# Kernel optimization log

Hardware: AMD Instinct MI355X
Metric: run time of the kernel (lower is better)

## Reference

```python
import jax, jax.numpy as jnp
import numpy as np

N, CIN, COUT, V, T, S = 32, 64, 128, 25, 300, 3  # batch, in/out channels, joints, frames, subsets
EPS = 1e-5  # torch BatchNorm2d default eps


def setup_inputs() -> dict:
    key = jax.random.key(0)
    ks = jax.random.split(key, 16)
    f = lambda i, shape, sc=1.0: jax.random.normal(ks[i], shape, jnp.float32) * sc
    return dict(
        x=f(0, (N, CIN, V, T)),            # forward arg: input features
        ada_A=f(1, (N, CIN, V, V), 0.1),   # forward arg: adaptive adjacency features
        PA=f(2, (S, V, V), 0.1),           # learned adjacency (adaptive=True)
        conv3_w=f(3, (S, COUT, CIN), 0.05),  # per-subset 1x1 conv weights
        conv3_b=f(4, (S, COUT), 0.01),
        ada_w=f(5, (S, COUT, CIN), 0.05),    # per-subset conv_ada weights
        ada_b=f(6, (S, COUT), 0.01),
        bn_gamma=jnp.ones((COUT,), jnp.float32),
        bn_beta=jnp.zeros((COUT,), jnp.float32),
        bn_mean=f(7, (COUT,), 0.01),
        bn_var=jnp.abs(f(8, (COUT,))) + 1.0,
        down_w=f(9, (COUT, CIN), 0.05),      # residual 1x1 conv (in_c != out_c)
        down_b=f(10, (COUT,), 0.01),
        dbn_gamma=jnp.ones((COUT,), jnp.float32),
        dbn_beta=jnp.zeros((COUT,), jnp.float32),
        dbn_mean=f(11, (COUT,), 0.01),
        dbn_var=jnp.abs(f(12, (COUT,))) + 1.0,
    )


def _bn(y, g, b, m, v):
    # inference-mode BatchNorm2d over channel axis 1; y: [N, C, V, T]
    scale = g * jax.lax.rsqrt(v + EPS)
    return (y - m[:, None, None]) * scale[:, None, None] + b[:, None, None]


def reference(x, ada_A, PA, conv3_w, conv3_b, ada_w, ada_b,
              bn_gamma, bn_beta, bn_mean, bn_var,
              down_w, down_b, dbn_gamma, dbn_beta, dbn_mean, dbn_var):
    # per-subset 1x1 conv on features: feat[s] = conv3_s(x)  -> [S, N, COUT, V, T]
    feat = jnp.einsum('nivt,soi->snovt', x, conv3_w) + conv3_b[:, None, :, None, None]
    # per-subset 1x1 conv on adjacency features -> [S, N, COUT, V, V]
    adaA = jnp.einsum('nivw,soi->snovw', ada_A, ada_w) + ada_b[:, None, :, None, None]
    # modulate by learned adjacency PA[s] broadcast over (batch, channel)
    A_full = adaA * PA[:, None, None, :, :]
    # graph matmul per subset + sum over subsets -> [N, COUT, V, T]
    out = jnp.einsum('snovw,snowt->novt', A_full, feat)
    out = _bn(out, bn_gamma, bn_beta, bn_mean, bn_var)
    # residual down-path: 1x1 conv + BN (in_c != out_c)
    res = jnp.einsum('nivt,oi->novt', x, down_w) + down_b[:, None, None]
    res = _bn(res, dbn_gamma, dbn_beta, dbn_mean, dbn_var)
    return jax.nn.relu(out + res)
```

## Files before the change

### kernel.cpp

```cpp
#include <hip/hip_runtime.h>
#include <stdint.h>

#define N_    32
#define CIN_  64
#define COUT_ 128
#define V_    25
#define T_    300
#define S_    3


using short8 = __attribute__((ext_vector_type(8))) short;
using f32x4  = __attribute__((ext_vector_type(4))) float;

#define MFMA(a, b, c) __builtin_amdgcn_mfma_f32_16x16x32_bf16(a, b, c, 0, 0, 0)

__device__ __forceinline__ float b2f(unsigned short u) {
  return __uint_as_float(((uint32_t)u) << 16);
}
__device__ __forceinline__ unsigned short f2b(float f) {
  uint32_t u = __float_as_uint(f);
  u += 0x7fffu + ((u >> 16) & 1u);
  return (unsigned short)(u >> 16);
}
template<bool ISB>
__device__ __forceinline__ float ldf(const void* p, int i) {
  return ISB ? b2f(((const unsigned short*)p)[i]) : ((const float*)p)[i];
}
__device__ __forceinline__ short8 zero8() {
  short8 z = {0, 0, 0, 0, 0, 0, 0, 0};
  return z;
}
__device__ __forceinline__ short8 ld_s8(const unsigned short* p, int st) {
  union { uint32_t u[4]; short8 s; } r;
  r.u[0] = (uint32_t)p[0]      | ((uint32_t)p[st]     << 16);
  r.u[1] = (uint32_t)p[2 * st] | ((uint32_t)p[3 * st] << 16);
  r.u[2] = (uint32_t)p[4 * st] | ((uint32_t)p[5 * st] << 16);
  r.u[3] = (uint32_t)p[6 * st] | ((uint32_t)p[7 * st] << 16);
  return r.s;
}
__device__ __forceinline__ short8 ld_f8h(const float* p, int st) {
  short8 r;
#pragma unroll
  for (int j = 0; j < 8; ++j) r[j] = (short)f2b(p[j * st]);
  return r;
}
__device__ __forceinline__ void ld_f8s(const float* p, int st,
                                       short8& h, short8& l) {
#pragma unroll
  for (int j = 0; j < 8; ++j) {
    float xv = p[j * st];
    unsigned short hu = f2b(xv);
    h[j] = (short)hu;
    l[j] = (short)f2b(xv - b2f(hu));
  }
}

__global__ void gcn_dtype_flag(const void* __restrict__ gamma, int* __restrict__ flag) {
  if (threadIdx.x == 0 && blockIdx.x == 0)
    flag[0] = (((const unsigned short*)gamma)[0] == 0x3F80u) ? 1 : 0;
}

__global__ __launch_bounds__(256) void tx_bf(
    const unsigned short* __restrict__ x, unsigned short* __restrict__ xt,
    const int* __restrict__ flag) {
  if (!flag || flag[0] == 0) return;
  __shared__ uint32_t til[64][151];
  const int b = blockIdx.x, n = b / 25, v = b % 25, tid = threadIdx.x;
  const unsigned short* xp = x + (size_t)n * 480000 + v * 300;
  for (int u = tid; u < 9600; u += 256) {
    const int i = u / 150, tp = u % 150;
    til[i][tp] = *(const uint32_t*)(xp + (size_t)i * 7500 + 2 * tp);
  }
  __syncthreads();
  unsigned short* op = xt + (size_t)n * 480000 + (size_t)v * 19200;
  for (int u = tid; u < 2400; u += 256) {
    const int t = u >> 3, oct = u & 7;
    uint32_t pk[4];
#pragma unroll
    for (int j = 0; j < 4; ++j) {
      const uint32_t w0 = til[oct * 8 + 2 * j][t >> 1];
      const uint32_t w1 = til[oct * 8 + 2 * j + 1][t >> 1];
      const uint32_t a = (t & 1) ? (w0 >> 16) : (w0 & 0xffffu);
      const uint32_t c = (t & 1) ? (w1 >> 16) : (w1 & 0xffffu);
      pk[j] = a | (c << 16);
    }
    *(uint4*)(op + t * 64 + oct * 8) = *(uint4*)pk;
  }
}

__global__ __launch_bounds__(256) void tx_f32(
    const float* __restrict__ x, unsigned short* __restrict__ xh,
    unsigned short* __restrict__ xl, const int* __restrict__ flag) {
  if (!flag || flag[0] != 0) return;
  __shared__ uint32_t til[64][303];
  const int b = blockIdx.x, n = b / 25, v = b % 25, tid = threadIdx.x;
  const float* xp = x + (size_t)n * 480000 + v * 300;
  for (int u = tid; u < 9600; u += 256) {
    const int i = u / 150, tp = u % 150;
    const float2 xv = *(const float2*)(xp + (size_t)i * 7500 + 2 * tp);
    unsigned short h0 = f2b(xv.x), h1 = f2b(xv.y);
    unsigned short l0 = f2b(xv.x - b2f(h0)), l1 = f2b(xv.y - b2f(h1));
    til[i][2 * tp]     = ((uint32_t)h0 << 16) | l0;
    til[i][2 * tp + 1] = ((uint32_t)h1 << 16) | l1;
  }
  __syncthreads();
  const size_t ob = (size_t)n * 480000 + (size_t)v * 19200;
  for (int u = tid; u < 2400; u += 256) {
    const int t = u >> 3, oct = u & 7;
    uint32_t w[8];
#pragma unroll
    for (int k = 0; k < 8; ++k) w[k] = til[oct * 8 + k][t];
    uint32_t ph[4], pl[4];
#pragma unroll
    for (int j = 0; j < 4; ++j) {
      ph[j] = (w[2 * j] >> 16) | (w[2 * j + 1] & 0xffff0000u);
      pl[j] = (w[2 * j] & 0xffffu) | (w[2 * j + 1] << 16);
    }
    *(uint4*)(xh + ob + t * 64 + oct * 8) = *(uint4*)ph;
    *(uint4*)(xl + ob + t * 64 + oct * 8) = *(uint4*)pl;
  }
}

template<bool ISB, bool TR>
__global__ __launch_bounds__(256, 4) void gcn_mfma(
    const void* __restrict__ x,    const void* __restrict__ ada,
    const void* __restrict__ PA,
    const void* __restrict__ c3w,  const void* __restrict__ c3b,
    const void* __restrict__ adw,  const void* __restrict__ adb,
    const void* __restrict__ bng,  const void* __restrict__ bnb,
    const void* __restrict__ bnm,  const void* __restrict__ bnv,
    const void* __restrict__ dww,  const void* __restrict__ dwb,
    const void* __restrict__ dbg,  const void* __restrict__ dbb,
    const void* __restrict__ dbm,  const void* __restrict__ dbv,
    void* __restrict__ out,
    const unsigned short* __restrict__ xt0,
    const unsigned short* __restrict__ xt1,
    const int* __restrict__ flag)
{
  if (ISB) { if (flag && flag[0] == 0) return; }
  else     { if (!flag || flag[0] != 0) return; }

  __shared__ __align__(16) unsigned char SM[37776];
  unsigned short* A_l = (unsigned short*)SM;
  float* resl = (float*)(SM + 24576);

  const int tid  = threadIdx.x;
  const int lane = tid & 63;
  const int tl   = lane & 15;
  const int khi  = lane >> 4;
  const int wv   = tid >> 6;

  const int b  = blockIdx.x;
  const int n  = (b & 7) * 4 + (b >> 8);
  const int o0 = ((b >> 3) & 31) * 4;

  const unsigned short* xnu   = (const unsigned short*)x   + (size_t)n * 480000;
  const float*          xnf   = (const float*)x            + (size_t)n * 480000;
  const unsigned short* adanu = (const unsigned short*)ada + (size_t)n * 40000;
  const float*          adanf = (const float*)ada          + (size_t)n * 40000;
  const unsigned short* xtn   = xt0 ? xt0 + (size_t)n * 480000 : nullptr;
  const unsigned short* xln   = xt1 ? xt1 + (size_t)n * 480000 : nullptr;

  float sc4[4];
#pragma unroll
  for (int o = 0; o < 4; ++o)
    sc4[o] = ldf<ISB>(bng, o0 + o) * rsqrtf(ldf<ISB>(bnv, o0 + o) + 1e-5f);
  const float dscv = ldf<ISB>(dbg, o0 + wv) * rsqrtf(ldf<ISB>(dbv, o0 + wv) + 1e-5f);
  const float c0v  = ldf<ISB>(bnb, o0 + wv) + ldf<ISB>(dbb, o0 + wv)
                   - ldf<ISB>(bnm, o0 + wv) * sc4[wv] - ldf<ISB>(dbm, o0 + wv) * dscv;

  short8 wb0, wb1, wb0l = zero8(), wb1l = zero8();
  if constexpr (ISB) {
    const unsigned short* wr = (tl < 12)
        ? (const unsigned short*)c3w + ((tl >> 2) * COUT_ + o0 + (tl & 3)) * CIN_
        : (const unsigned short*)dww + (o0 + (tl & 3)) * CIN_;
    wb0 = *(const short8*)(wr + khi * 8);
    wb1 = *(const short8*)(wr + 32 + khi * 8);
  } else {
    const float* wr = (tl < 12)
        ? (const float*)c3w + ((tl >> 2) * COUT_ + o0 + (tl & 3)) * CIN_
        : (const float*)dww + (o0 + (tl & 3)) * CIN_;
    ld_f8s(wr + khi * 8,      1, wb0, wb0l);
    ld_f8s(wr + 32 + khi * 8, 1, wb1, wb1l);
  }
  f32x4 fbias;
#pragma unroll
  for (int rg = 0; rg < 4; ++rg)
    fbias[rg] = (khi < 3) ? ldf<ISB>(c3b, khi * COUT_ + o0 + rg)
                          : ldf<ISB>(dwb, o0 + rg);

  for (int e = tid; e < 4800; e += 256) ((float*)SM)[e] = 0.f;
  __syncthreads();
  {
    short8 aw0 = zero8(), aw1 = zero8();
    if (tl < 12) {
      if constexpr (ISB) {
        const unsigned short* ar = (const unsigned short*)adw
            + ((tl >> 2) * COUT_ + o0 + (tl & 3)) * CIN_;
        aw0 = *(const short8*)(ar + khi * 8);
        aw1 = *(const short8*)(ar + 32 + khi * 8);
      } else {
        const float* ar = (const float*)adw
            + ((tl >> 2) * COUT_ + o0 + (tl & 3)) * CIN_;
        aw0 = ld_f8h(ar + khi * 8, 1);
        aw1 = ld_f8h(ar + 32 + khi * 8, 1);
      }
    }
    f32x4 ab;
#pragma unroll
    for (int rg = 0; rg < 4; ++rg)
      ab[rg] = (khi < 3) ? ldf<ISB>(adb, khi * COUT_ + o0 + rg) : 0.f;

    for (int ti = wv * 10; ti < wv * 10 + 10; ++ti) {
      const int pos = ti * 16 + tl;
      const bool pv = pos < 625;
      short8 bf0 = zero8(), bf1 = zero8();
      if (pv) {
        if constexpr (ISB) {
          bf0 = ld_s8(adanu + (khi * 8) * 625 + pos, 625);
          bf1 = ld_s8(adanu + (32 + khi * 8) * 625 + pos, 625);
        } else {
          bf0 = ld_f8h(adanf + (khi * 8) * 625 + pos, 625);
          bf1 = ld_f8h(adanf + (32 + khi * 8) * 625 + pos, 625);
        }
      }
      f32x4 acc = ab;
      acc = MFMA(aw0, bf0, acc);
      acc = MFMA(aw1, bf1, acc);
      if (pv && khi < 3) {
        const int vv = pos / 25, ww = pos % 25;
        const float pa = ldf<ISB>(PA, khi * 625 + pos);
#pragma unroll
        for (int rg = 0; rg < 4; ++rg)
          A_l[((rg * 3 + khi) * 25 + vv) * 32 + ww] = f2b(acc[rg] * pa * sc4[rg]);
      }
    }
  }
  __syncthreads();

  short8 afr[3][2];
#pragma unroll
  for (int s = 0; s < 3; ++s) {
    afr[s][0] = *(const short8*)(A_l + ((wv * 3 + s) * 25 + tl) * 32 + khi * 8);
    afr[s][1] = (tl < 9)
        ? *(const short8*)(A_l + ((wv * 3 + s) * 25 + 16 + tl) * 32 + khi * 8)
        : zero8();
  }
  __syncthreads();

  for (int e = tid; e < 6144; e += 256) ((float*)SM)[e] = 0.f;
  __syncthreads();

  const int wlo = wv * 6;
  const int whi = (wv == 3) ? 25 : wv * 6 + 6;

  for (int ch = 0; ch < 10; ++ch) {
    const int t0 = ch * 32;

    if constexpr (ISB) {
      for (int w = wlo; w < whi; w += 2) {
        const bool pr = (w + 1 < whi);
#pragma unroll
        for (int nt = 0; nt < 2; ++nt) {
          const int tlc = nt * 16 + tl;
          const int t = t0 + tlc;
          short8 a0 = zero8(), a1 = zero8(), b0 = zero8(), b1 = zero8();
          if (t < 300) {
            if constexpr (TR) {
              const unsigned short* p = xtn + ((size_t)(w * 300 + t) << 6);
              a0 = *(const short8*)(p + khi * 8);
              a1 = *(const short8*)(p + 32 + khi * 8);
              if (pr) {
                b0 = *(const short8*)(p + 19200 + khi * 8);
                b1 = *(const short8*)(p + 19200 + 32 + khi * 8);
              }
            } else {
              const unsigned short* p = xnu + (khi * 8) * 7500 + w * 300 + t;
              a0 = ld_s8(p, 7500);
              a1 = ld_s8(p + 32 * 7500, 7500);
              if (pr) {
                b0 = ld_s8(p + 300, 7500);
                b1 = ld_s8(p + 300 + 32 * 7500, 7500);
              }
            }
          }
          f32x4 fA = fbias, fB = fbias;
          fA = MFMA(wb0, a0, fA);
          fA = MFMA(wb1, a1, fA);
          fB = MFMA(wb0, b0, fB);
          fB = MFMA(wb1, b1, fB);
          if (khi == 3) {
#pragma unroll
            for (int rg = 0; rg < 4; ++rg) {
              resl[(rg * 25 + w) * 33 + tlc] = fA[rg];
              if (pr) resl[(rg * 25 + w + 1) * 33 + tlc] = fB[rg];
            }
          } else {
            const int sb = ((((w >> 3) ^ (tl & 3) ^ khi) & 3) << 4) + (w & 7) * 2;
            if (pr) {
#pragma unroll
              for (int rg = 0; rg < 4; ++rg)
                *(uint32_t*)(SM + (khi * 4 + rg) * 2048 + tlc * 64 + sb)
                    = (uint32_t)f2b(fA[rg]) | ((uint32_t)f2b(fB[rg]) << 16);
            } else {
#pragma unroll
              for (int rg = 0; rg < 4; ++rg)
                *(unsigned short*)(SM + (khi * 4 + rg) * 2048 + tlc * 64 + sb)
                    = f2b(fA[rg]);
            }
          }
        }
      }
    } else {
      for (int w = wlo; w < whi; ++w) {
#pragma unroll
        for (int nt = 0; nt < 2; ++nt) {
          const int tlc = nt * 16 + tl;
          const int t = t0 + tlc;
          short8 h0 = zero8(), h1 = zero8(), l0 = zero8(), l1 = zero8();
          if (t < 300) {
            if constexpr (TR) {
              const size_t off = (size_t)(w * 300 + t) << 6;
              h0 = *(const short8*)(xtn + off + khi * 8);
              h1 = *(const short8*)(xtn + off + 32 + khi * 8);
              l0 = *(const short8*)(xln + off + khi * 8);
              l1 = *(const short8*)(xln + off + 32 + khi * 8);
            } else {
              const float* p = xnf + (khi * 8) * 7500 + w * 300 + t;
              ld_f8s(p, 7500, h0, l0);
              ld_f8s(p + 32 * 7500, 7500, h1, l1);
            }
          }
          f32x4 f = fbias, g = {0.f, 0.f, 0.f, 0.f};
          f = MFMA(wb0, h0, f);
          f = MFMA(wb1, h1, f);
          g = MFMA(wb0, l0, g);
          g = MFMA(wb1, l1, g);
          g = MFMA(wb0l, h0, g);
          g = MFMA(wb1l, h1, g);
          f = f + g;
          if (khi == 3) {
#pragma unroll
            for (int rg = 0; rg < 4; ++rg)
              resl[(rg * 25 + w) * 33 + tlc] = f[rg];
          } else {
            const int sb = ((((w >> 3) ^ (tl & 3) ^ khi) & 3) << 4) + (w & 7) * 2;
#pragma unroll
            for (int rg = 0; rg < 4; ++rg)
              *(unsigned short*)(SM + (khi * 4 + rg) * 2048 + tlc * 64 + sb)
                  = f2b(f[rg]);
          }
        }
      }
    }
    __syncthreads();

#pragma unroll
    for (int nt = 0; nt < 2; ++nt) {
      const int tlc = nt * 16 + tl;
      const int t = t0 + tlc;
      f32x4 d0 = {0.f, 0.f, 0.f, 0.f};
      f32x4 d1 = {0.f, 0.f, 0.f, 0.f};
#pragma unroll
      for (int s = 0; s < 3; ++s) {
        const int row = s * 4 + wv;
        const short8 bf = *(const short8*)(
            SM + row * 2048 + tlc * 64 + (((khi ^ (tlc & 3) ^ s) & 3) << 4));
        d0 = MFMA(afr[s][0], bf, d0);
        d1 = MFMA(afr[s][1], bf, d1);
      }
      if (t < 300) {
        const int obase = (n * COUT_ + o0 + wv) * 7500 + t;
#pragma unroll
        for (int rg = 0; rg < 4; ++rg) {
          const int v0 = khi * 4 + rg;
          const float y0 = fmaxf(
              d0[rg] + resl[(wv * 25 + v0) * 33 + tlc] * dscv + c0v, 0.f);
          if constexpr (ISB) ((unsigned short*)out)[obase + v0 * 300] = f2b(y0);
          else               ((float*)out)[obase + v0 * 300] = y0;
          const int v1 = 16 + v0;
          if (v1 < 25) {
            const float y1 = fmaxf(
                d1[rg] + resl[(wv * 25 + v1) * 33 + tlc] * dscv + c0v, 0.f);
            if constexpr (ISB) ((unsigned short*)out)[obase + v1 * 300] = f2b(y1);
            else               ((float*)out)[obase + v1 * 300] = y1;
          }
        }
      }
    }
    __syncthreads();
  }
}

extern "C" void kernel_launch(void* const* d_in, const int* in_sizes, int n_in,
                              void* d_out, int out_size, void* d_ws, size_t ws_size,
                              hipStream_t stream) {
  const size_t PL = 30720000;
  int* flag = (ws_size >= sizeof(int)) ? (int*)d_ws : nullptr;
  unsigned short* P0 = (unsigned short*)((char*)d_ws + 1024);
  unsigned short* P1 = (unsigned short*)((char*)d_ws + 1024 + PL);
  const bool trb = flag && ws_size >= 1024 + PL;
  const bool trf = flag && ws_size >= 1024 + 2 * PL;

  if (flag) gcn_dtype_flag<<<1, 64, 0, stream>>>(d_in[7], flag);
  if (trb) tx_bf<<<dim3(800), 256, 0, stream>>>(
      (const unsigned short*)d_in[0], P0, flag);
  if (trf) tx_f32<<<dim3(800), 256, 0, stream>>>(
      (const float*)d_in[0], P0, P1, flag);

  if (trb)
    gcn_mfma<true, true><<<dim3(1024), 256, 0, stream>>>(
        d_in[0], d_in[1], d_in[2], d_in[3], d_in[4], d_in[5], d_in[6],
        d_in[7], d_in[8], d_in[9], d_in[10], d_in[11], d_in[12],
        d_in[13], d_in[14], d_in[15], d_in[16], d_out, P0, nullptr, flag);
  else
    gcn_mfma<true, false><<<dim3(1024), 256, 0, stream>>>(
        d_in[0], d_in[1], d_in[2], d_in[3], d_in[4], d_in[5], d_in[6],
        d_in[7], d_in[8], d_in[9], d_in[10], d_in[11], d_in[12],
        d_in[13], d_in[14], d_in[15], d_in[16], d_out, nullptr, nullptr, flag);

  if (flag) {
    if (trf)
      gcn_mfma<false, true><<<dim3(1024), 256, 0, stream>>>(
          d_in[0], d_in[1], d_in[2], d_in[3], d_in[4], d_in[5], d_in[6],
          d_in[7], d_in[8], d_in[9], d_in[10], d_in[11], d_in[12],
          d_in[13], d_in[14], d_in[15], d_in[16], d_out, P0, P1, flag);
    else
      gcn_mfma<false, false><<<dim3(1024), 256, 0, stream>>>(
          d_in[0], d_in[1], d_in[2], d_in[3], d_in[4], d_in[5], d_in[6],
          d_in[7], d_in[8], d_in[9], d_in[10], d_in[11], d_in[12],
          d_in[13], d_in[14], d_in[15], d_in[16], d_out, nullptr, nullptr, flag);
  }
}
```

Measured before the change: 496.6 us.

## Keep per-wave feature tiles in registers and drop per-chunk block barriers

The main loop now assigns each wave its own 16-frame tiles. The conv3 outputs for all 25 joints are packed directly into MFMA B-operand registers (pbv) instead of being staged through shared memory, so the per-chunk __syncthreads pairs disappear. The adjacency matrix is stored in a swizzled 128-wide layout covering all three subsets, and each wave handles all four output channels per tile. The residual values go into a per-wave float4 LDS region. In exchange, register pressure and LDS per block go up, and occupancy drops from 4 to 2 blocks per CU.

Result: slower. 602.5 us (+21.3%).

```diff
diff --git a/kernel.cpp b/kernel.cpp
--- a/kernel.cpp
+++ b/kernel.cpp
@@ -122,7 +122,7 @@
 }
 
 template<bool ISB, bool TR>
-__global__ __launch_bounds__(256, 4) void gcn_mfma(
+__global__ __launch_bounds__(256, 2) void gcn_mfma(
     const void* __restrict__ x,    const void* __restrict__ ada,
     const void* __restrict__ PA,
     const void* __restrict__ c3w,  const void* __restrict__ c3b,
@@ -140,9 +140,9 @@
   if (ISB) { if (flag && flag[0] == 0) return; }
   else     { if (!flag || flag[0] != 0) return; }
 
-  __shared__ __align__(16) unsigned char SM[37776];
+  __shared__ __align__(16) unsigned char SM[52800];
   unsigned short* A_l = (unsigned short*)SM;
-  float* resl = (float*)(SM + 24576);
+  float* resl = (float*)(SM + 25600);
 
   const int tid  = threadIdx.x;
   const int lane = tid & 63;
@@ -161,13 +161,14 @@
   const unsigned short* xtn   = xt0 ? xt0 + (size_t)n * 480000 : nullptr;
   const unsigned short* xln   = xt1 ? xt1 + (size_t)n * 480000 : nullptr;
 
-  float sc4[4];
-#pragma unroll
-  for (int o = 0; o < 4; ++o)
-    sc4[o] = ldf<ISB>(bng, o0 + o) * rsqrtf(ldf<ISB>(bnv, o0 + o) + 1e-5f);
-  const float dscv = ldf<ISB>(dbg, o0 + wv) * rsqrtf(ldf<ISB>(dbv, o0 + wv) + 1e-5f);
-  const float c0v  = ldf<ISB>(bnb, o0 + wv) + ldf<ISB>(dbb, o0 + wv)
-                   - ldf<ISB>(bnm, o0 + wv) * sc4[wv] - ldf<ISB>(dbm, o0 + wv) * dscv;
+  float sc4[4], dsc4[4], c04[4];
+#pragma unroll
+  for (int o = 0; o < 4; ++o) {
+    sc4[o]  = ldf<ISB>(bng, o0 + o) * rsqrtf(ldf<ISB>(bnv, o0 + o) + 1e-5f);
+    dsc4[o] = ldf<ISB>(dbg, o0 + o) * rsqrtf(ldf<ISB>(dbv, o0 + o) + 1e-5f);
+    c04[o]  = ldf<ISB>(bnb, o0 + o) + ldf<ISB>(dbb, o0 + o)
+            - ldf<ISB>(bnm, o0 + o) * sc4[o] - ldf<ISB>(dbm, o0 + o) * dsc4[o];
+  }
 
   short8 wb0, wb1, wb0l = zero8(), wb1l = zero8();
   if constexpr (ISB) {
@@ -189,7 +190,7 @@
     fbias[rg] = (khi < 3) ? ldf<ISB>(c3b, khi * COUT_ + o0 + rg)
                           : ldf<ISB>(dwb, o0 + rg);
 
-  for (int e = tid; e < 4800; e += 256) ((float*)SM)[e] = 0.f;
+  for (int e = tid; e < 6400; e += 256) ((float*)SM)[e] = 0.f;
   __syncthreads();
   {
     short8 aw0 = zero8(), aw1 = zero8();
@@ -232,93 +233,46 @@
         const float pa = ldf<ISB>(PA, khi * 625 + pos);
 #pragma unroll
         for (int rg = 0; rg < 4; ++rg)
-          A_l[((rg * 3 + khi) * 25 + vv) * 32 + ww] = f2b(acc[rg] * pa * sc4[rg]);
+          A_l[((rg * 25 + vv) << 7) + ((khi * 32 + ww) ^ ((vv & 7) << 3))]
+              = f2b(acc[rg] * pa * sc4[rg]);
       }
     }
   }
   __syncthreads();
 
-  short8 afr[3][2];
-#pragma unroll
-  for (int s = 0; s < 3; ++s) {
-    afr[s][0] = *(const short8*)(A_l + ((wv * 3 + s) * 25 + tl) * 32 + khi * 8);
-    afr[s][1] = (tl < 9)
-        ? *(const short8*)(A_l + ((wv * 3 + s) * 25 + 16 + tl) * 32 + khi * 8)
-        : zero8();
-  }
-  __syncthreads();
-
-  for (int e = tid; e < 6144; e += 256) ((float*)SM)[e] = 0.f;
-  __syncthreads();
-
-  const int wlo = wv * 6;
-  const int whi = (wv == 3) ? 25 : wv * 6 + 6;
-
-  for (int ch = 0; ch < 10; ++ch) {
-    const int t0 = ch * 32;
-
-    if constexpr (ISB) {
-      for (int w = wlo; w < whi; w += 2) {
-        const bool pr = (w + 1 < whi);
-#pragma unroll
-        for (int nt = 0; nt < 2; ++nt) {
-          const int tlc = nt * 16 + tl;
-          const int t = t0 + tlc;
-          short8 a0 = zero8(), a1 = zero8(), b0 = zero8(), b1 = zero8();
-          if (t < 300) {
+  for (int tg = wv; tg < 19; tg += 4) {
+    const int t  = tg * 16 + tl;
+    const bool tv = t < 300;
+
+    short8 pbv[4][4];
+#pragma unroll
+    for (int oo = 0; oo < 4; ++oo) pbv[oo][3] = zero8();
+
+#pragma unroll
+    for (int g = 0; g < 4; ++g) {
+#pragma unroll
+      for (int j = 0; j < 8; ++j) {
+        const int w = g * 8 + j;
+        if (w >= 25) continue;
+        f32x4 f = fbias;
+        if constexpr (ISB) {
+          short8 a0 = zero8(), a1 = zero8();
+          if (tv) {
             if constexpr (TR) {
               const unsigned short* p = xtn + ((size_t)(w * 300 + t) << 6);
               a0 = *(const short8*)(p + khi * 8);
               a1 = *(const short8*)(p + 32 + khi * 8);
-              if (pr) {
-                b0 = *(const short8*)(p + 19200 + khi * 8);
-                b1 = *(const short8*)(p + 19200 + 32 + khi * 8);
-              }
             } else {
               const unsigned short* p = xnu + (khi * 8) * 7500 + w * 300 + t;
               a0 = ld_s8(p, 7500);
               a1 = ld_s8(p + 32 * 7500, 7500);
-              if (pr) {
-                b0 = ld_s8(p + 300, 7500);
-                b1 = ld_s8(p + 300 + 32 * 7500, 7500);
-              }
             }
           }
-          f32x4 fA = fbias, fB = fbias;
-          fA = MFMA(wb0, a0, fA);
-          fA = MFMA(wb1, a1, fA);
-          fB = MFMA(wb0, b0, fB);
-          fB = MFMA(wb1, b1, fB);
-          if (khi == 3) {
-#pragma unroll
-            for (int rg = 0; rg < 4; ++rg) {
-              resl[(rg * 25 + w) * 33 + tlc] = fA[rg];
-              if (pr) resl[(rg * 25 + w + 1) * 33 + tlc] = fB[rg];
-            }
-          } else {
-            const int sb = ((((w >> 3) ^ (tl & 3) ^ khi) & 3) << 4) + (w & 7) * 2;
-            if (pr) {
-#pragma unroll
-              for (int rg = 0; rg < 4; ++rg)
-                *(uint32_t*)(SM + (khi * 4 + rg) * 2048 + tlc * 64 + sb)
-                    = (uint32_t)f2b(fA[rg]) | ((uint32_t)f2b(fB[rg]) << 16);
-            } else {
-#pragma unroll
-              for (int rg = 0; rg < 4; ++rg)
-                *(unsigned short*)(SM + (khi * 4 + rg) * 2048 + tlc * 64 + sb)
-                    = f2b(fA[rg]);
-            }
-          }
-        }
-      }
-    } else {
-      for (int w = wlo; w < whi; ++w) {
-#pragma unroll
-        for (int nt = 0; nt < 2; ++nt) {
-          const int tlc = nt * 16 + tl;
-          const int t = t0 + tlc;
+          f = MFMA(wb0, a0, f);
+          f = MFMA(wb1, a1, f);
+        } else {
           short8 h0 = zero8(), h1 = zero8(), l0 = zero8(), l1 = zero8();
-          if (t < 300) {
+          if (tv) {
             if constexpr (TR) {
               const size_t off = (size_t)(w * 300 + t) << 6;
               h0 = *(const short8*)(xtn + off + khi * 8);
@@ -331,64 +285,56 @@
               ld_f8s(p + 32 * 7500, 7500, h1, l1);
             }
           }
-          f32x4 f = fbias, g = {0.f, 0.f, 0.f, 0.f};
-          f = MFMA(wb0, h0, f);
-          f = MFMA(wb1, h1, f);
-          g = MFMA(wb0, l0, g);
-          g = MFMA(wb1, l1, g);
-          g = MFMA(wb0l, h0, g);
-          g = MFMA(wb1l, h1, g);
-          f = f + g;
-          if (khi == 3) {
-#pragma unroll
-            for (int rg = 0; rg < 4; ++rg)
-              resl[(rg * 25 + w) * 33 + tlc] = f[rg];
-          } else {
-            const int sb = ((((w >> 3) ^ (tl & 3) ^ khi) & 3) << 4) + (w & 7) * 2;
-#pragma unroll
-            for (int rg = 0; rg < 4; ++rg)
-              *(unsigned short*)(SM + (khi * 4 + rg) * 2048 + tlc * 64 + sb)
-                  = f2b(f[rg]);
-          }
+          f32x4 gg = {0.f, 0.f, 0.f, 0.f};
+          f  = MFMA(wb0, h0, f);
+          f  = MFMA(wb1, h1, f);
+          gg = MFMA(wb0, l0, gg);
+          gg = MFMA(wb1, l1, gg);
+          gg = MFMA(wb0l, h0, gg);
+          gg = MFMA(wb1l, h1, gg);
+          f = f + gg;
         }
-      }
-    }
-    __syncthreads();
-
-#pragma unroll
-    for (int nt = 0; nt < 2; ++nt) {
-      const int tlc = nt * 16 + tl;
-      const int t = t0 + tlc;
+        if (khi == 3)
+          *(f32x4*)&resl[(wv * 25 + w) * 68 + tl * 4] = f;
+#pragma unroll
+        for (int oo = 0; oo < 4; ++oo)
+          pbv[oo][g][j] = (short)f2b(f[oo]);
+      }
+    }
+
+#pragma unroll
+    for (int oo = 0; oo < 4; ++oo) {
       f32x4 d0 = {0.f, 0.f, 0.f, 0.f};
       f32x4 d1 = {0.f, 0.f, 0.f, 0.f};
 #pragma unroll
-      for (int s = 0; s < 3; ++s) {
-        const int row = s * 4 + wv;
-        const short8 bf = *(const short8*)(
-            SM + row * 2048 + tlc * 64 + (((khi ^ (tlc & 3) ^ s) & 3) << 4));
-        d0 = MFMA(afr[s][0], bf, d0);
-        d1 = MFMA(afr[s][1], bf, d1);
-      }
-      if (t < 300) {
-        const int obase = (n * COUT_ + o0 + wv) * 7500 + t;
+      for (int g = 0; g < 4; ++g) {
+        const int x0 = (khi * 32 + g * 8) ^ ((tl & 7) << 3);
+        const short8 af0 = *(const short8*)(A_l + ((oo * 25 + tl) << 7) + x0);
+        short8 af1 = zero8();
+        if (tl < 9)
+          af1 = *(const short8*)(A_l + ((oo * 25 + 16 + tl) << 7) + x0);
+        d0 = MFMA(af0, pbv[oo][g], d0);
+        d1 = MFMA(af1, pbv[oo][g], d1);
+      }
+      if (tv) {
+        const int obase = (n * COUT_ + o0 + oo) * 7500 + t;
 #pragma unroll
         for (int rg = 0; rg < 4; ++rg) {
           const int v0 = khi * 4 + rg;
-          const float y0 = fmaxf(
-              d0[rg] + resl[(wv * 25 + v0) * 33 + tlc] * dscv + c0v, 0.f);
+          const f32x4 rv0 = *(const f32x4*)&resl[(wv * 25 + v0) * 68 + tl * 4];
+          const float y0 = fmaxf(d0[rg] + rv0[oo] * dsc4[oo] + c04[oo], 0.f);
           if constexpr (ISB) ((unsigned short*)out)[obase + v0 * 300] = f2b(y0);
           else               ((float*)out)[obase + v0 * 300] = y0;
           const int v1 = 16 + v0;
           if (v1 < 25) {
-            const float y1 = fmaxf(
-                d1[rg] + resl[(wv * 25 + v1) * 33 + tlc] * dscv + c0v, 0.f);
+            const f32x4 rv1 = *(const f32x4*)&resl[(wv * 25 + v1) * 68 + tl * 4];
+            const float y1 = fmaxf(d1[rg] + rv1[oo] * dsc4[oo] + c04[oo], 0.f);
             if constexpr (ISB) ((unsigned short*)out)[obase + v1 * 300] = f2b(y1);
             else               ((float*)out)[obase + v1 * 300] = y1;
           }
         }
       }
     }
-    __syncthreads();
   }
 }
 
```

## Software-pipeline transposed-input loads in GCN MFMA kernel and peel tail chunk

Applied to the files above, without the earlier changes.

For the transposed-input paths, the per-chunk feature conv is restructured so the next tile's global loads are issued before the current tile's MFMAs run (double-buffered registers). Joint assignment moves from contiguous ranges to strided interleaving, and the last partial chunk is peeled off so the main loop drops its t<300 bounds checks. Launch bounds go from 4 to 3 waves per SIMD, leaving the compiler more registers for the extra live buffers at the cost of occupancy.

Result: slower. 623.1 us (+25.5%).

```diff
diff --git a/kernel.cpp b/kernel.cpp
--- a/kernel.cpp
+++ b/kernel.cpp
@@ -122,7 +122,7 @@
 }
 
 template<bool ISB, bool TR>
-__global__ __launch_bounds__(256, 4) void gcn_mfma(
+__global__ __launch_bounds__(256, 3) void gcn_mfma(
     const void* __restrict__ x,    const void* __restrict__ ada,
     const void* __restrict__ PA,
     const void* __restrict__ c3w,  const void* __restrict__ c3b,
@@ -251,114 +251,13 @@
   for (int e = tid; e < 6144; e += 256) ((float*)SM)[e] = 0.f;
   __syncthreads();
 
-  const int wlo = wv * 6;
-  const int whi = (wv == 3) ? 25 : wv * 6 + 6;
-
-  for (int ch = 0; ch < 10; ++ch) {
-    const int t0 = ch * 32;
-
-    if constexpr (ISB) {
-      for (int w = wlo; w < whi; w += 2) {
-        const bool pr = (w + 1 < whi);
-#pragma unroll
-        for (int nt = 0; nt < 2; ++nt) {
-          const int tlc = nt * 16 + tl;
-          const int t = t0 + tlc;
-          short8 a0 = zero8(), a1 = zero8(), b0 = zero8(), b1 = zero8();
-          if (t < 300) {
-            if constexpr (TR) {
-              const unsigned short* p = xtn + ((size_t)(w * 300 + t) << 6);
-              a0 = *(const short8*)(p + khi * 8);
-              a1 = *(const short8*)(p + 32 + khi * 8);
-              if (pr) {
-                b0 = *(const short8*)(p + 19200 + khi * 8);
-                b1 = *(const short8*)(p + 19200 + 32 + khi * 8);
-              }
-            } else {
-              const unsigned short* p = xnu + (khi * 8) * 7500 + w * 300 + t;
-              a0 = ld_s8(p, 7500);
-              a1 = ld_s8(p + 32 * 7500, 7500);
-              if (pr) {
-                b0 = ld_s8(p + 300, 7500);
-                b1 = ld_s8(p + 300 + 32 * 7500, 7500);
-              }
-            }
-          }
-          f32x4 fA = fbias, fB = fbias;
-          fA = MFMA(wb0, a0, fA);
-          fA = MFMA(wb1, a1, fA);
-          fB = MFMA(wb0, b0, fB);
-          fB = MFMA(wb1, b1, fB);
-          if (khi == 3) {
-#pragma unroll
-            for (int rg = 0; rg < 4; ++rg) {
-              resl[(rg * 25 + w) * 33 + tlc] = fA[rg];
-              if (pr) resl[(rg * 25 + w + 1) * 33 + tlc] = fB[rg];
-            }
-          } else {
-            const int sb = ((((w >> 3) ^ (tl & 3) ^ khi) & 3) << 4) + (w & 7) * 2;
-            if (pr) {
-#pragma unroll
-              for (int rg = 0; rg < 4; ++rg)
-                *(uint32_t*)(SM + (khi * 4 + rg) * 2048 + tlc * 64 + sb)
-                    = (uint32_t)f2b(fA[rg]) | ((uint32_t)f2b(fB[rg]) << 16);
-            } else {
-#pragma unroll
-              for (int rg = 0; rg < 4; ++rg)
-                *(unsigned short*)(SM + (khi * 4 + rg) * 2048 + tlc * 64 + sb)
-                    = f2b(fA[rg]);
-            }
-          }
-        }
-      }
-    } else {
-      for (int w = wlo; w < whi; ++w) {
-#pragma unroll
-        for (int nt = 0; nt < 2; ++nt) {
-          const int tlc = nt * 16 + tl;
-          const int t = t0 + tlc;
-          short8 h0 = zero8(), h1 = zero8(), l0 = zero8(), l1 = zero8();
-          if (t < 300) {
-            if constexpr (TR) {
-              const size_t off = (size_t)(w * 300 + t) << 6;
-              h0 = *(const short8*)(xtn + off + khi * 8);
-              h1 = *(const short8*)(xtn + off + 32 + khi * 8);
-              l0 = *(const short8*)(xln + off + khi * 8);
-              l1 = *(const short8*)(xln + off + 32 + khi * 8);
-            } else {
-              const float* p = xnf + (khi * 8) * 7500 + w * 300 + t;
-              ld_f8s(p, 7500, h0, l0);
-              ld_f8s(p + 32 * 7500, 7500, h1, l1);
-            }
-          }
-          f32x4 f = fbias, g = {0.f, 0.f, 0.f, 0.f};
-          f = MFMA(wb0, h0, f);
-          f = MFMA(wb1, h1, f);
-          g = MFMA(wb0, l0, g);
-          g = MFMA(wb1, l1, g);
-          g = MFMA(wb0l, h0, g);
-          g = MFMA(wb1l, h1, g);
-          f = f + g;
-          if (khi == 3) {
-#pragma unroll
-            for (int rg = 0; rg < 4; ++rg)
-              resl[(rg * 25 + w) * 33 + tlc] = f[rg];
-          } else {
-            const int sb = ((((w >> 3) ^ (tl & 3) ^ khi) & 3) << 4) + (w & 7) * 2;
-#pragma unroll
-            for (int rg = 0; rg < 4; ++rg)
-              *(unsigned short*)(SM + (khi * 4 + rg) * 2048 + tlc * 64 + sb)
-                  = f2b(f[rg]);
-          }
-        }
-      }
-    }
-    __syncthreads();
-
+  auto phaseC = [&](int t0, bool tailg) {
 #pragma unroll
     for (int nt = 0; nt < 2; ++nt) {
+      const int tt = t0 + nt * 16;
+      if (tailg && tt >= 300) continue;
       const int tlc = nt * 16 + tl;
-      const int t = t0 + tlc;
+      const int t = tt + tl;
       f32x4 d0 = {0.f, 0.f, 0.f, 0.f};
       f32x4 d1 = {0.f, 0.f, 0.f, 0.f};
 #pragma unroll
@@ -369,7 +268,7 @@
         d0 = MFMA(afr[s][0], bf, d0);
         d1 = MFMA(afr[s][1], bf, d1);
       }
-      if (t < 300) {
+      if (!tailg || t < 300) {
         const int obase = (n * COUT_ + o0 + wv) * 7500 + t;
 #pragma unroll
         for (int rg = 0; rg < 4; ++rg) {
@@ -388,7 +287,299 @@
         }
       }
     }
-    __syncthreads();
+  };
+
+  if constexpr (TR) {
+    if constexpr (ISB) {
+      auto LDP = [&](short8& A0, short8& A1, short8& B0, short8& B1,
+                     int w, int t) {
+        const unsigned short* p = xtn + (((size_t)(w * 300 + t)) << 6);
+        A0 = *(const short8*)(p + khi * 8);
+        A1 = *(const short8*)(p + 32 + khi * 8);
+        B0 = *(const short8*)(p + 19200 + khi * 8);
+        B1 = *(const short8*)(p + 19200 + 32 + khi * 8);
+      };
+      auto CMPP = [&](short8 A0, short8 A1, short8 B0, short8 B1,
+                      int w, int tlc) {
+        f32x4 fA = fbias, fB = fbias;
+        fA = MFMA(wb0, A0, fA);
+        fA = MFMA(wb1, A1, fA);
+        fB = MFMA(wb0, B0, fB);
+        fB = MFMA(wb1, B1, fB);
+        if (khi == 3) {
+#pragma unroll
+          for (int rg = 0; rg < 4; ++rg) {
+            resl[(rg * 25 + w) * 33 + tlc]     = fA[rg];
+            resl[(rg * 25 + w + 1) * 33 + tlc] = fB[rg];
+          }
+        } else {
+          const int sb = ((((w >> 3) ^ (tl & 3) ^ khi) & 3) << 4) + (w & 7) * 2;
+#pragma unroll
+          for (int rg = 0; rg < 4; ++rg)
+            *(uint32_t*)(SM + (khi * 4 + rg) * 2048 + tlc * 64 + sb)
+                = (uint32_t)f2b(fA[rg]) | ((uint32_t)f2b(fB[rg]) << 16);
+        }
+      };
+      const int w0 = 2 * wv, w1 = w0 + 8, w2 = w0 + 16;
+      short8 pa0, pa1, pb0, pb1, qa0, qa1, qb0, qb1;
+      LDP(pa0, pa1, pb0, pb1, w0, tl);
+      for (int ch = 0; ch < 9; ++ch) {
+        const int t0 = ch * 32;
+        LDP(qa0, qa1, qb0, qb1, w0, t0 + 16 + tl);
+        CMPP(pa0, pa1, pb0, pb1, w0, tl);
+        LDP(pa0, pa1, pb0, pb1, w1, t0 + tl);
+        CMPP(qa0, qa1, qb0, qb1, w0, 16 + tl);
+        LDP(qa0, qa1, qb0, qb1, w1, t0 + 16 + tl);
+        CMPP(pa0, pa1, pb0, pb1, w1, tl);
+        LDP(pa0, pa1, pb0, pb1, w2, t0 + tl);
+        CMPP(qa0, qa1, qb0, qb1, w1, 16 + tl);
+        LDP(qa0, qa1, qb0, qb1, w2, t0 + 16 + tl);
+        CMPP(pa0, pa1, pb0, pb1, w2, tl);
+        LDP(pa0, pa1, pb0, pb1, w0, t0 + 32 + tl);
+        CMPP(qa0, qa1, qb0, qb1, w2, 16 + tl);
+        if (wv == 0) {
+#pragma unroll
+          for (int nt = 0; nt < 2; ++nt) {
+            const int tlc = nt * 16 + tl;
+            const unsigned short* p =
+                xtn + (((size_t)(24 * 300 + t0 + tlc)) << 6);
+            short8 a0 = *(const short8*)(p + khi * 8);
+            short8 a1 = *(const short8*)(p + 32 + khi * 8);
+            f32x4 f = fbias;
+            f = MFMA(wb0, a0, f);
+            f = MFMA(wb1, a1, f);
+            if (khi == 3) {
+#pragma unroll
+              for (int rg = 0; rg < 4; ++rg)
+                resl[(rg * 25 + 24) * 33 + tlc] = f[rg];
+            } else {
+              const int sb = (((3 ^ (tl & 3) ^ khi) & 3) << 4);
+#pragma unroll
+              for (int rg = 0; rg < 4; ++rg)
+                *(unsigned short*)(SM + (khi * 4 + rg) * 2048 + tlc * 64 + sb)
+                    = f2b(f[rg]);
+            }
+          }
+        }
+        __syncthreads();
+        phaseC(t0, false);
+        __syncthreads();
+      }
+      {
+        const int t = 288 + tl;
+        const bool lv = t < 300;
+#pragma unroll
+        for (int pi = 0; pi < 3; ++pi) {
+          const int w = 2 * wv + 8 * pi;
+          short8 a0 = zero8(), a1 = zero8(), b0 = zero8(), b1 = zero8();
+          if (lv) LDP(a0, a1, b0, b1, w, t);
+          CMPP(a0, a1, b0, b1, w, tl);
+        }
+        if (wv == 0) {
+          short8 a0 = zero8(), a1 = zero8();
+          if (lv) {
+            const unsigned short* p = xtn + (((size_t)(24 * 300 + t)) << 6);
+            a0 = *(const short8*)(p + khi * 8);
+            a1 = *(const short8*)(p + 32 + khi * 8);
+          }
+          f32x4 f = fbias;
+          f = MFMA(wb0, a0, f);
+          f = MFMA(wb1, a1, f);
+          if (khi == 3) {
+#pragma unroll
+            for (int rg = 0; rg < 4; ++rg)
+              resl[(rg * 25 + 24) * 33 + tl] = f[rg];
+          } else {
+            const int sb = (((3 ^ (tl & 3) ^ khi) & 3) << 4);
+#pragma unroll
+            for (int rg = 0; rg < 4; ++rg)
+              *(unsigned short*)(SM + (khi * 4 + rg) * 2048 + tl * 64 + sb)
+                  = f2b(f[rg]);
+          }
+        }
+        __syncthreads();
+        phaseC(288, true);
+      }
+    } else {
+      auto LD4 = [&](short8& H0, short8& H1, short8& L0, short8& L1,
+                     int w, int t) {
+        const size_t off = ((size_t)(w * 300 + t)) << 6;
+        H0 = *(const short8*)(xtn + off + khi * 8);
+        H1 = *(const short8*)(xtn + off + 32 + khi * 8);
+        L0 = *(const short8*)(xln + off + khi * 8);
+        L1 = *(const short8*)(xln + off + 32 + khi * 8);
+      };
+      auto CMP4 = [&](short8 H0, short8 H1, short8 L0, short8 L1,
+                      int w, int tlc) {
+        f32x4 f = fbias, g = {0.f, 0.f, 0.f, 0.f};
+        f = MFMA(wb0, H0, f);
+        f = MFMA(wb1, H1, f);
+        g = MFMA(wb0, L0, g);
+        g = MFMA(wb1, L1, g);
+        g = MFMA(wb0l, H0, g);
+        g = MFMA(wb1l, H1, g);
+        f = f + g;
+        if (khi == 3) {
+#pragma unroll
+          for (int rg = 0; rg < 4; ++rg)
+            resl[(rg * 25 + w) * 33 + tlc] = f[rg];
+        } else {
+          const int sb = ((((w >> 3) ^ (tl & 3) ^ khi) & 3) << 4) + (w & 7) * 2;
+#pragma unroll
+          for (int rg = 0; rg < 4; ++rg)
+            *(unsigned short*)(SM + (khi * 4 + rg) * 2048 + tlc * 64 + sb)
+                = f2b(f[rg]);
+        }
+      };
+      const int w0 = wv, w1 = wv + 4, w2 = wv + 8,
+                w3 = wv + 12, w4 = wv + 16, w5 = wv + 20;
+      short8 ph0, ph1, pl0, pl1, qh0, qh1, ql0, ql1;
+      LD4(ph0, ph1, pl0, pl1, w0, tl);
+      for (int ch = 0; ch < 9; ++ch) {
+        const int t0 = ch * 32;
+        LD4(qh0, qh1, ql0, ql1, w0, t0 + 16 + tl);
+        CMP4(ph0, ph1, pl0, pl1, w0, tl);
+        LD4(ph0, ph1, pl0, pl1, w1, t0 + tl);
+        CMP4(qh0, qh1, ql0, ql1, w0, 16 + tl);
+        LD4(qh0, qh1, ql0, ql1, w1, t0 + 16 + tl);
+        CMP4(ph0, ph1, pl0, pl1, w1, tl);
+        LD4(ph0, ph1, pl0, pl1, w2, t0 + tl);
+        CMP4(qh0, qh1, ql0, ql1, w1, 16 + tl);
+        LD4(qh0, qh1, ql0, ql1, w2, t0 + 16 + tl);
+        CMP4(ph0, ph1, pl0, pl1, w2, tl);
+        LD4(ph0, ph1, pl0, pl1, w3, t0 + tl);
+        CMP4(qh0, qh1, ql0, ql1, w2, 16 + tl);
+        LD4(qh0, qh1, ql0, ql1, w3, t0 + 16 + tl);
+        CMP4(ph0, ph1, pl0, pl1, w3, tl);
+        LD4(ph0, ph1, pl0, pl1, w4, t0 + tl);
+        CMP4(qh0, qh1, ql0, ql1, w3, 16 + tl);
+        LD4(qh0, qh1, ql0, ql1, w4, t0 + 16 + tl);
+        CMP4(ph0, ph1, pl0, pl1, w4, tl);
+        LD4(ph0, ph1, pl0, pl1, w5, t0 + tl);
+        CMP4(qh0, qh1, ql0, ql1, w4, 16 + tl);
+        LD4(qh0, qh1, ql0, ql1, w5, t0 + 16 + tl);
+        CMP4(ph0, ph1, pl0, pl1, w5, tl);
+        LD4(ph0, ph1, pl0, pl1, w0, t0 + 32 + tl);
+        CMP4(qh0, qh1, ql0, ql1, w5, 16 + tl);
+        if (wv == 0) {
+#pragma unroll
+          for (int nt = 0; nt < 2; ++nt) {
+            const int tlc = nt * 16 + tl;
+            short8 h0, h1, l0, l1;
+            LD4(h0, h1, l0, l1, 24, t0 + tlc);
+            CMP4(h0, h1, l0, l1, 24, tlc);
+          }
+        }
+        __syncthreads();
+        phaseC(t0, false);
+        __syncthreads();
+      }
+      {
+        const int t = 288 + tl;
+        const bool lv = t < 300;
+#pragma unroll
+        for (int i = 0; i < 6; ++i) {
+          const int w = wv + 4 * i;
+          short8 h0 = zero8(), h1 = zero8(), l0 = zero8(), l1 = zero8();
+          if (lv) LD4(h0, h1, l0, l1, w, t);
+          CMP4(h0, h1, l0, l1, w, tl);
+        }
+        if (wv == 0) {
+          short8 h0 = zero8(), h1 = zero8(), l0 = zero8(), l1 = zero8();
+          if (lv) LD4(h0, h1, l0, l1, 24, t);
+          CMP4(h0, h1, l0, l1, 24, tl);
+        }
+        __syncthreads();
+        phaseC(288, true);
+      }
+    }
+  } else {
+    const int wlo = wv * 6;
+    const int whi = (wv == 3) ? 25 : wv * 6 + 6;
+    for (int ch = 0; ch < 10; ++ch) {
+      const int t0 = ch * 32;
+      if constexpr (ISB) {
+        for (int w = wlo; w < whi; w += 2) {
+          const bool pr = (w + 1 < whi);
+#pragma unroll
+          for (int nt = 0; nt < 2; ++nt) {
+            const int tlc = nt * 16 + tl;
+            const int t = t0 + tlc;
+            short8 a0 = zero8(), a1 = zero8(), b0 = zero8(), b1 = zero8();
+            if (t < 300) {
+              const unsigned short* p = xnu + (khi * 8) * 7500 + w * 300 + t;
+              a0 = ld_s8(p, 7500);
+              a1 = ld_s8(p + 32 * 7500, 7500);
+              if (pr) {
+                b0 = ld_s8(p + 300, 7500);
+                b1 = ld_s8(p + 300 + 32 * 7500, 7500);
+              }
+            }
+            f32x4 fA = fbias, fB = fbias;
+            fA = MFMA(wb0, a0, fA);
+            fA = MFMA(wb1, a1, fA);
+            fB = MFMA(wb0, b0, fB);
+            fB = MFMA(wb1, b1, fB);
+            if (khi == 3) {
+#pragma unroll
+              for (int rg = 0; rg < 4; ++rg) {
+                resl[(rg * 25 + w) * 33 + tlc] = fA[rg];
+                if (pr) resl[(rg * 25 + w + 1) * 33 + tlc] = fB[rg];
+              }
+            } else {
+              const int sb = ((((w >> 3) ^ (tl & 3) ^ khi) & 3) << 4) + (w & 7) * 2;
+              if (pr) {
+#pragma unroll
+                for (int rg = 0; rg < 4; ++rg)
+                  *(uint32_t*)(SM + (khi * 4 + rg) * 2048 + tlc * 64 + sb)
+                      = (uint32_t)f2b(fA[rg]) | ((uint32_t)f2b(fB[rg]) << 16);
+              } else {
+#pragma unroll
+                for (int rg = 0; rg < 4; ++rg)
+                  *(unsigned short*)(SM + (khi * 4 + rg) * 2048 + tlc * 64 + sb)
+                      = f2b(fA[rg]);
+              }
+            }
+          }
+        }
+      } else {
+        for (int w = wlo; w < whi; ++w) {
+#pragma unroll
+          for (int nt = 0; nt < 2; ++nt) {
+            const int tlc = nt * 16 + tl;
+            const int t = t0 + tlc;
+            short8 h0 = zero8(), h1 = zero8(), l0 = zero8(), l1 = zero8();
+            if (t < 300) {
+              const float* p = xnf + (khi * 8) * 7500 + w * 300 + t;
+              ld_f8s(p, 7500, h0, l0);
+              ld_f8s(p + 32 * 7500, 7500, h1, l1);
+            }
+            f32x4 f = fbias, g = {0.f, 0.f, 0.f, 0.f};
+            f = MFMA(wb0, h0, f);
+            f = MFMA(wb1, h1, f);
+            g = MFMA(wb0, l0, g);
+            g = MFMA(wb1, l1, g);
+            g = MFMA(wb0l, h0, g);
+            g = MFMA(wb1l, h1, g);
+            f = f + g;
+            if (khi == 3) {
+#pragma unroll
+              for (int rg = 0; rg < 4; ++rg)
+                resl[(rg * 25 + w) * 33 + tlc] = f[rg];
+            } else {
+              const int sb = ((((w >> 3) ^ (tl & 3) ^ khi) & 3) << 4) + (w & 7) * 2;
+#pragma unroll
+              for (int rg = 0; rg < 4; ++rg)
+                *(unsigned short*)(SM + (khi * 4 + rg) * 2048 + tlc * 64 + sb)
+                    = f2b(f[rg]);
+            }
+          }
+        }
+      }
+      __syncthreads();
+      phaseC(t0, true);
+      __syncthreads();
+    }
   }
 }
 
```
